# Kernel optimization log

Hardware: AMD Instinct MI355X
Metric: run time of the kernel (lower is better)

The kernel has to match this reference:

```python
import jax, jax.numpy as jnp
import numpy as np

INPUT_SIZE = 1024
HEAD_SIZE = 64


def setup_inputs() -> dict:
    key = jax.random.key(0)
    kx, kk, kq, kv = jax.random.split(key, 4)
    B, T, C, H = 4, 4096, INPUT_SIZE, HEAD_SIZE
    x = jax.random.normal(kx, (B, T, C), dtype=jnp.float32)
    # nn.Linear(C, H, bias=False) weight is (H, C); we store transposed (C, H)
    # so that y = x @ W matches torch's x @ weight.T
    scale = 1.0 / np.sqrt(C)
    Wk = jax.random.uniform(kk, (C, H), dtype=jnp.float32, minval=-scale, maxval=scale)
    Wq = jax.random.uniform(kq, (C, H), dtype=jnp.float32, minval=-scale, maxval=scale)
    Wv = jax.random.uniform(kv, (C, H), dtype=jnp.float32, minval=-scale, maxval=scale)
    return {"x": x, "Wk": Wk, "Wq": Wq, "Wv": Wv}


def reference(x, Wk, Wq, Wv):
    B, T, C = x.shape
    k = x @ Wk  # (B, T, H)
    q = x @ Wq
    v = x @ Wv
    H = k.shape[-1]
    # scaled scores (B, T, T)
    wei = jnp.einsum('bth,bsh->bts', q, k) * (H ** -0.5)
    causal = jnp.tril(jnp.ones((T, T), dtype=bool))
    wei = jnp.where(causal, wei, -jnp.inf)
    wei = jax.nn.softmax(wei, axis=-1)
    out = jnp.einsum('bts,bsh->bth', wei, v)  # (B, T, H)
    return out
```

## Files before the change

kernel.cpp:

```cpp
#include <hip/hip_runtime.h>
#include <math.h>


#define BT   16384
#define TDIM 4096
#define CDIM 1024
#define HDIM 64
#define ACCW 68
#define NSLOT 288

typedef __attribute__((ext_vector_type(8))) short bf16x8;
typedef __attribute__((ext_vector_type(4))) float f32x4;
typedef __attribute__((ext_vector_type(8))) unsigned short us8;
typedef __attribute__((ext_vector_type(4))) unsigned short us4;

static __device__ __forceinline__ unsigned short f2bf(float f) {
    unsigned int u = __float_as_uint(f);
    u += 0x7fffu + ((u >> 16) & 1u);
    return (unsigned short)(u >> 16);
}

static __device__ __forceinline__ void pswap(unsigned &x, unsigned &y) {
    asm("v_permlane32_swap_b32 %0, %1" : "+v"(x), "+v"(y));
    asm("v_permlane16_swap_b32 %0, %1" : "+v"(x), "+v"(y));
}

__global__ __launch_bounds__(256) void wtrans(
    const float* __restrict__ Wk, const float* __restrict__ Wq,
    const float* __restrict__ Wv, unsigned short* __restrict__ wtg)
{
    int idx = blockIdx.x * 256 + threadIdx.x;
    int mat = idx >> 16;
    int rem = idx & 65535;
    int h = rem >> 10, c = rem & 1023;
    const float* W = (mat == 0) ? Wk : (mat == 1) ? Wq : Wv;
    wtg[idx] = f2bf(W[c * HDIM + h]);
}

__global__ __launch_bounds__(512) void qkv_proj(
    const float* __restrict__ x, const unsigned short* __restrict__ wtg,
    unsigned short* __restrict__ kg, unsigned short* __restrict__ qg,
    unsigned short* __restrict__ vtg)
{
    __shared__ __align__(16) unsigned short xs[2][32][72];
    __shared__ __align__(16) unsigned short wts[2][192][72];
    const int t = threadIdx.x;
    const int lane = t & 63, wv = t >> 6, quad = lane >> 4, l16 = lane & 15;
    const int mt = wv >> 2;
    const int nq = wv & 3;
    const int row0 = blockIdx.x * 32;

    const int xr = t >> 4, xc4 = (t & 15) * 4;
    const int wn = t >> 3, wc8 = (t & 7) * 8;

    f32x4 acc3[3];
    #pragma unroll
    for (int i = 0; i < 3; i++) acc3[i] = (f32x4){0.f, 0.f, 0.f, 0.f};

    const size_t xrow = (size_t)(row0 + xr) * CDIM + xc4;

    float4 xv = *(const float4*)&x[xrow];
    us8 w0 = *(const us8*)&wtg[(size_t)(wn +   0) * CDIM + wc8];
    us8 w1 = *(const us8*)&wtg[(size_t)(wn +  64) * CDIM + wc8];
    us8 w2 = *(const us8*)&wtg[(size_t)(wn + 128) * CDIM + wc8];
    {
        us4 pk = { f2bf(xv.x), f2bf(xv.y), f2bf(xv.z), f2bf(xv.w) };
        *(us4*)&xs[0][xr][xc4] = pk;
        *(us8*)&wts[0][wn +   0][wc8] = w0;
        *(us8*)&wts[0][wn +  64][wc8] = w1;
        *(us8*)&wts[0][wn + 128][wc8] = w2;
    }
    xv = *(const float4*)&x[xrow + 64];
    w0 = *(const us8*)&wtg[(size_t)(wn +   0) * CDIM + 64 + wc8];
    w1 = *(const us8*)&wtg[(size_t)(wn +  64) * CDIM + 64 + wc8];
    w2 = *(const us8*)&wtg[(size_t)(wn + 128) * CDIM + 64 + wc8];
    __syncthreads();

    for (int it = 0; it < 16; it++) {
        const int buf = it & 1;
        if (it + 1 < 16) {
            us4 pk = { f2bf(xv.x), f2bf(xv.y), f2bf(xv.z), f2bf(xv.w) };
            *(us4*)&xs[buf ^ 1][xr][xc4] = pk;
            *(us8*)&wts[buf ^ 1][wn +   0][wc8] = w0;
            *(us8*)&wts[buf ^ 1][wn +  64][wc8] = w1;
            *(us8*)&wts[buf ^ 1][wn + 128][wc8] = w2;
            if (it + 2 < 16) {
                int nc = (it + 2) * 64;
                xv = *(const float4*)&x[xrow + nc];
                w0 = *(const us8*)&wtg[(size_t)(wn +   0) * CDIM + nc + wc8];
                w1 = *(const us8*)&wtg[(size_t)(wn +  64) * CDIM + nc + wc8];
                w2 = *(const us8*)&wtg[(size_t)(wn + 128) * CDIM + nc + wc8];
            }
        }
        bf16x8 a0 = *(const bf16x8*)&xs[buf][mt * 16 + l16][quad * 8];
        bf16x8 a1 = *(const bf16x8*)&xs[buf][mt * 16 + l16][32 + quad * 8];
        #pragma unroll
        for (int j = 0; j < 3; j++) {
            int nt = nq * 3 + j;
            bf16x8 b0 = *(const bf16x8*)&wts[buf][nt * 16 + l16][quad * 8];
            bf16x8 b1 = *(const bf16x8*)&wts[buf][nt * 16 + l16][32 + quad * 8];
            acc3[j] = __builtin_amdgcn_mfma_f32_16x16x32_bf16(a0, b0, acc3[j], 0, 0, 0);
            acc3[j] = __builtin_amdgcn_mfma_f32_16x16x32_bf16(a1, b1, acc3[j], 0, 0, 0);
        }
        __syncthreads();
    }

    const int mrow = row0 + mt * 16 + quad * 4;
    #pragma unroll
    for (int j = 0; j < 3; j++) {
        int nt = nq * 3 + j;
        int mat = nt >> 2;
        int col = (nt & 3) * 16 + l16;
        if (mat == 2) {
            int bb = mrow >> 12, tr = mrow & 4095;
            us4 pv = { f2bf(acc3[j][0]), f2bf(acc3[j][1]),
                       f2bf(acc3[j][2]), f2bf(acc3[j][3]) };
            *(us4*)&vtg[((size_t)(bb * HDIM + col) << 12) + tr] = pv;
        } else {
            float s = (mat == 1) ? 0.125f : 1.0f;
            unsigned short* dst = (mat == 0) ? kg : qg;
            #pragma unroll
            for (int reg = 0; reg < 4; reg++)
                dst[(size_t)(mrow + reg) * HDIM + col] = f2bf(acc3[j][reg] * s);
        }
    }
}

__global__ __launch_bounds__(256) void attn(
    const unsigned short* __restrict__ qg, const unsigned short* __restrict__ kg,
    const unsigned short* __restrict__ vtg, float* __restrict__ slabs)
{
    __shared__ __align__(16) unsigned short Ks[2][64][72];
    __shared__ __align__(16) unsigned short Vt[2][64][72];

    const int t = threadIdx.x;
    const int lane = t & 63, wv = t >> 6, quad = lane >> 4, l16 = lane & 15;

    const int b = blockIdx.x / NSLOT;
    const int s = blockIdx.x - b * NSLOT;
    int a;
    if      (s < 8)   a = 0;
    else if (s < 24)  a = 1;
    else if (s < 48)  a = 2;
    else if (s < 80)  a = 3;
    else if (s < 120) a = 4;
    else if (s < 168) a = 5;
    else if (s < 224) a = 6;
    else              a = 7;
    const int u  = s - 4 * a * (a + 1);
    const int qt = a * 8 + u / (a + 1);
    const int c  = u % (a + 1);

    const size_t bbase = (size_t)b * TDIM;
    const int Q0 = qt * 64;
    const int kt0 = c * 8;
    const int kt1 = (kt0 + 7 < qt) ? kt0 + 7 : qt;

    const int qrow = Q0 + wv * 16 + l16;
    const bf16x8 qa0 = *(const bf16x8*)&qg[(bbase + qrow) * HDIM + quad * 8];
    const bf16x8 qa1 = *(const bf16x8*)&qg[(bbase + qrow) * HDIM + 32 + quad * 8];

    const short onev = (l16 == 0) ? (short)0x3F80 : (short)0;
    const bf16x8 ones = { onev, onev, onev, onev, onev, onev, onev, onev };

    f32x4 O[5];
    #pragma unroll
    for (int i = 0; i < 5; i++) O[i] = (f32x4){0.f, 0.f, 0.f, 0.f};

    const int fr = t >> 3, fc = (t & 7) * 8;

    us8 kr0 = *(const us8*)&kg[(bbase + kt0 * 64 + fr) * HDIM + fc];
    us8 kr1 = *(const us8*)&kg[(bbase + kt0 * 64 + fr + 32) * HDIM + fc];
    us8 vr0 = *(const us8*)&vtg[((size_t)(b * HDIM + fr) << 12) + kt0 * 64 + fc];
    us8 vr1 = *(const us8*)&vtg[((size_t)(b * HDIM + fr + 32) << 12) + kt0 * 64 + fc];
    *(us8*)&Ks[0][fr][fc] = kr0;
    *(us8*)&Ks[0][fr + 32][fc] = kr1;
    *(us8*)&Vt[0][fr][fc] = vr0;
    *(us8*)&Vt[0][fr + 32][fc] = vr1;
    if (kt0 < kt1) {
        int kn = kt0 + 1;
        kr0 = *(const us8*)&kg[(bbase + kn * 64 + fr) * HDIM + fc];
        kr1 = *(const us8*)&kg[(bbase + kn * 64 + fr + 32) * HDIM + fc];
        vr0 = *(const us8*)&vtg[((size_t)(b * HDIM + fr) << 12) + kn * 64 + fc];
        vr1 = *(const us8*)&vtg[((size_t)(b * HDIM + fr + 32) << 12) + kn * 64 + fc];
    }
    __syncthreads();

    const int qloc = wv * 16 + l16;
    int buf = 0;
    for (int kt = kt0; kt <= kt1; kt++) {
        f32x4 sT[4];
        #pragma unroll
        for (int st = 0; st < 4; st++) {
            bf16x8 kb0 = *(const bf16x8*)&Ks[buf][st * 16 + l16][quad * 8];
            bf16x8 kb1 = *(const bf16x8*)&Ks[buf][st * 16 + l16][32 + quad * 8];
            f32x4 z = (f32x4){0.f, 0.f, 0.f, 0.f};
            z = __builtin_amdgcn_mfma_f32_16x16x32_bf16(kb0, qa0, z, 0, 0, 0);
            z = __builtin_amdgcn_mfma_f32_16x16x32_bf16(kb1, qa1, z, 0, 0, 0);
            sT[st] = z;
        }

        if (kt < kt1) {
            *(us8*)&Ks[buf ^ 1][fr][fc] = kr0;
            *(us8*)&Ks[buf ^ 1][fr + 32][fc] = kr1;
            *(us8*)&Vt[buf ^ 1][fr][fc] = vr0;
            *(us8*)&Vt[buf ^ 1][fr + 32][fc] = vr1;
            if (kt + 1 < kt1) {
                int kn = kt + 2;
                kr0 = *(const us8*)&kg[(bbase + kn * 64 + fr) * HDIM + fc];
                kr1 = *(const us8*)&kg[(bbase + kn * 64 + fr + 32) * HDIM + fc];
                vr0 = *(const us8*)&vtg[((size_t)(b * HDIM + fr) << 12) + kn * 64 + fc];
                vr1 = *(const us8*)&vtg[((size_t)(b * HDIM + fr + 32) << 12) + kn * 64 + fc];
            }
        }

        float p[4][4];
        if (kt == qt) {
            #pragma unroll
            for (int st = 0; st < 4; st++)
                #pragma unroll
                for (int r = 0; r < 4; r++) {
                    int kkloc = st * 16 + quad * 4 + r;
                    p[st][r] = (kkloc > qloc) ? 0.f : __expf(sT[st][r]);
                }
        } else {
            #pragma unroll
            for (int st = 0; st < 4; st++)
                #pragma unroll
                for (int r = 0; r < 4; r++)
                    p[st][r] = __expf(sT[st][r]);
        }

        unsigned cpk[4][2];
        #pragma unroll
        for (int st = 0; st < 4; st++) {
            asm("v_cvt_pk_bf16_f32 %0, %1, %2"
                : "=v"(cpk[st][0]) : "v"(p[st][0]), "v"(p[st][1]));
            asm("v_cvt_pk_bf16_f32 %0, %1, %2"
                : "=v"(cpk[st][1]) : "v"(p[st][2]), "v"(p[st][3]));
        }
        union { unsigned u[4]; bf16x8 v; } pa0u, pa1u;
        {
            unsigned a0 = cpk[0][0], b0 = cpk[1][0]; pswap(a0, b0);
            unsigned a1 = cpk[0][1], b1 = cpk[1][1]; pswap(a1, b1);
            pa0u.u[0] = a0; pa0u.u[1] = a1; pa0u.u[2] = b0; pa0u.u[3] = b1;
            unsigned a2 = cpk[2][0], b2 = cpk[3][0]; pswap(a2, b2);
            unsigned a3 = cpk[2][1], b3 = cpk[3][1]; pswap(a3, b3);
            pa1u.u[0] = a2; pa1u.u[1] = a3; pa1u.u[2] = b2; pa1u.u[3] = b3;
        }
        const bf16x8 pa0 = pa0u.v, pa1 = pa1u.v;

        #pragma unroll
        for (int nt = 0; nt < 4; nt++) {
            bf16x8 vb0 = *(const bf16x8*)&Vt[buf][nt * 16 + l16][quad * 8];
            bf16x8 vb1 = *(const bf16x8*)&Vt[buf][nt * 16 + l16][32 + quad * 8];
            O[nt] = __builtin_amdgcn_mfma_f32_16x16x32_bf16(pa0, vb0, O[nt], 0, 0, 0);
            O[nt] = __builtin_amdgcn_mfma_f32_16x16x32_bf16(pa1, vb1, O[nt], 0, 0, 0);
        }
        O[4] = __builtin_amdgcn_mfma_f32_16x16x32_bf16(pa0, ones, O[4], 0, 0, 0);
        O[4] = __builtin_amdgcn_mfma_f32_16x16x32_bf16(pa1, ones, O[4], 0, 0, 0);

        __syncthreads();
        buf ^= 1;
    }

    float* slab = slabs + (size_t)(b * NSLOT + s) * 64 * ACCW;
    const int rl = wv * 16 + quad * 4;
    #pragma unroll
    for (int nt = 0; nt < 4; nt++)
        #pragma unroll
        for (int r = 0; r < 4; r++)
            slab[(size_t)(rl + r) * ACCW + nt * 16 + l16] = O[nt][r];
    if (l16 == 0) {
        #pragma unroll
        for (int r = 0; r < 4; r++)
            slab[(size_t)(rl + r) * ACCW + 64] = O[4][r];
    }
}

__global__ __launch_bounds__(256) void reduce_norm(
    const float* __restrict__ slabs, float* __restrict__ out)
{
    int idx = blockIdx.x * 256 + threadIdx.x;
    int row = idx >> 4, c4 = (idx & 15) * 4;
    int b = row >> 12, qt = (row >> 6) & 63, r64 = row & 63;
    int a = qt >> 3, nc = a + 1;
    int base = 4 * a * (a + 1) + (qt & 7) * nc;

    const float* sl = slabs + ((size_t)(b * NSLOT + base) * 64 + r64) * ACCW;
    float4 o = make_float4(0.f, 0.f, 0.f, 0.f);
    float l = 0.f;
    for (int i = 0; i < nc; i++) {
        float4 v = *(const float4*)&sl[c4];
        o.x += v.x; o.y += v.y; o.z += v.z; o.w += v.w;
        l += sl[64];
        sl += (size_t)64 * ACCW;
    }
    float inv = 1.f / l;
    *(float4*)&out[(size_t)row * HDIM + c4] =
        make_float4(o.x * inv, o.y * inv, o.z * inv, o.w * inv);
}

extern "C" void kernel_launch(void* const* d_in, const int* in_sizes, int n_in,
                              void* d_out, int out_size, void* d_ws, size_t ws_size,
                              hipStream_t stream) {
    const float* x  = (const float*)d_in[0];
    const float* Wk = (const float*)d_in[1];
    const float* Wq = (const float*)d_in[2];
    const float* Wv = (const float*)d_in[3];
    float* out = (float*)d_out;

    unsigned short* wtg = (unsigned short*)d_ws;
    unsigned short* kg  = wtg + 196608;
    unsigned short* qg  = kg + (size_t)BT * HDIM;
    unsigned short* vtg = qg + (size_t)BT * HDIM;
    float* slabs = (float*)(vtg + (size_t)4 * HDIM * TDIM);

    wtrans<<<768, 256, 0, stream>>>(Wk, Wq, Wv, wtg);
    qkv_proj<<<BT / 32, 512, 0, stream>>>(x, wtg, kg, qg, vtg);
    attn<<<4 * NSLOT, 256, 0, stream>>>(qg, kg, vtg, slabs);
    reduce_norm<<<BT * HDIM / (4 * 256), 256, 0, stream>>>(slabs, out);
}
```

Baseline: 141.9 us.

## Process 128 query rows per attention block and retile QKV projection

The attention kernel now handles two 64-row query tiles per block, so each K/V tile loaded into shared memory feeds both query groups. The work split changes to 4 key tiles per chunk, with a new slot decomposition found by a small search loop, and the reduction kernel is updated to match. The projection kernel moves to 256 threads with a 32-wide K step, where each wave computes two M tiles that share B operands, and occupancy hints are added to both kernels. The trade-off is higher register pressure from the doubled accumulators, plus a different load balance across blocks.

```diff
diff --git a/kernel.cpp b/kernel.cpp
--- a/kernel.cpp
+++ b/kernel.cpp
@@ -7,7 +7,7 @@
 #define CDIM 1024
 #define HDIM 64
 #define ACCW 68
-#define NSLOT 288
+#define NSLOT 272
 
 typedef __attribute__((ext_vector_type(8))) short bf16x8;
 typedef __attribute__((ext_vector_type(4))) float f32x4;
@@ -37,96 +37,100 @@
     wtg[idx] = f2bf(W[c * HDIM + h]);
 }
 
-__global__ __launch_bounds__(512) void qkv_proj(
+__global__ __launch_bounds__(256, 4) void qkv_proj(
     const float* __restrict__ x, const unsigned short* __restrict__ wtg,
     unsigned short* __restrict__ kg, unsigned short* __restrict__ qg,
     unsigned short* __restrict__ vtg)
 {
-    __shared__ __align__(16) unsigned short xs[2][32][72];
-    __shared__ __align__(16) unsigned short wts[2][192][72];
+    __shared__ __align__(16) unsigned short xs[2][32][36];
+    __shared__ __align__(16) unsigned short wts[2][192][36];
     const int t = threadIdx.x;
     const int lane = t & 63, wv = t >> 6, quad = lane >> 4, l16 = lane & 15;
-    const int mt = wv >> 2;
-    const int nq = wv & 3;
     const int row0 = blockIdx.x * 32;
 
-    const int xr = t >> 4, xc4 = (t & 15) * 4;
-    const int wn = t >> 3, wc8 = (t & 7) * 8;
-
-    f32x4 acc3[3];
+    const int xr = t >> 3, xc4 = (t & 7) * 4;
+    const int wr0 = t >> 2,          wc0 = (t & 3) * 8;
+    const int wr1 = (t + 256) >> 2,  wc1 = wc0;
+    const int wr2 = (t + 512) >> 2,  wc2 = wc0;
+
+    f32x4 acc[2][3];
     #pragma unroll
-    for (int i = 0; i < 3; i++) acc3[i] = (f32x4){0.f, 0.f, 0.f, 0.f};
+    for (int m = 0; m < 2; m++)
+        #pragma unroll
+        for (int j = 0; j < 3; j++) acc[m][j] = (f32x4){0.f, 0.f, 0.f, 0.f};
 
     const size_t xrow = (size_t)(row0 + xr) * CDIM + xc4;
 
     float4 xv = *(const float4*)&x[xrow];
-    us8 w0 = *(const us8*)&wtg[(size_t)(wn +   0) * CDIM + wc8];
-    us8 w1 = *(const us8*)&wtg[(size_t)(wn +  64) * CDIM + wc8];
-    us8 w2 = *(const us8*)&wtg[(size_t)(wn + 128) * CDIM + wc8];
+    us8 w0 = *(const us8*)&wtg[(size_t)wr0 * CDIM + wc0];
+    us8 w1 = *(const us8*)&wtg[(size_t)wr1 * CDIM + wc1];
+    us8 w2 = *(const us8*)&wtg[(size_t)wr2 * CDIM + wc2];
     {
         us4 pk = { f2bf(xv.x), f2bf(xv.y), f2bf(xv.z), f2bf(xv.w) };
         *(us4*)&xs[0][xr][xc4] = pk;
-        *(us8*)&wts[0][wn +   0][wc8] = w0;
-        *(us8*)&wts[0][wn +  64][wc8] = w1;
-        *(us8*)&wts[0][wn + 128][wc8] = w2;
-    }
-    xv = *(const float4*)&x[xrow + 64];
-    w0 = *(const us8*)&wtg[(size_t)(wn +   0) * CDIM + 64 + wc8];
-    w1 = *(const us8*)&wtg[(size_t)(wn +  64) * CDIM + 64 + wc8];
-    w2 = *(const us8*)&wtg[(size_t)(wn + 128) * CDIM + 64 + wc8];
+        *(us8*)&wts[0][wr0][wc0] = w0;
+        *(us8*)&wts[0][wr1][wc1] = w1;
+        *(us8*)&wts[0][wr2][wc2] = w2;
+    }
+    xv = *(const float4*)&x[xrow + 32];
+    w0 = *(const us8*)&wtg[(size_t)wr0 * CDIM + 32 + wc0];
+    w1 = *(const us8*)&wtg[(size_t)wr1 * CDIM + 32 + wc1];
+    w2 = *(const us8*)&wtg[(size_t)wr2 * CDIM + 32 + wc2];
     __syncthreads();
 
-    for (int it = 0; it < 16; it++) {
+    for (int it = 0; it < 32; it++) {
         const int buf = it & 1;
-        if (it + 1 < 16) {
+        if (it + 1 < 32) {
             us4 pk = { f2bf(xv.x), f2bf(xv.y), f2bf(xv.z), f2bf(xv.w) };
             *(us4*)&xs[buf ^ 1][xr][xc4] = pk;
-            *(us8*)&wts[buf ^ 1][wn +   0][wc8] = w0;
-            *(us8*)&wts[buf ^ 1][wn +  64][wc8] = w1;
-            *(us8*)&wts[buf ^ 1][wn + 128][wc8] = w2;
-            if (it + 2 < 16) {
-                int nc = (it + 2) * 64;
+            *(us8*)&wts[buf ^ 1][wr0][wc0] = w0;
+            *(us8*)&wts[buf ^ 1][wr1][wc1] = w1;
+            *(us8*)&wts[buf ^ 1][wr2][wc2] = w2;
+            if (it + 2 < 32) {
+                int nc = (it + 2) * 32;
                 xv = *(const float4*)&x[xrow + nc];
-                w0 = *(const us8*)&wtg[(size_t)(wn +   0) * CDIM + nc + wc8];
-                w1 = *(const us8*)&wtg[(size_t)(wn +  64) * CDIM + nc + wc8];
-                w2 = *(const us8*)&wtg[(size_t)(wn + 128) * CDIM + nc + wc8];
-            }
-        }
-        bf16x8 a0 = *(const bf16x8*)&xs[buf][mt * 16 + l16][quad * 8];
-        bf16x8 a1 = *(const bf16x8*)&xs[buf][mt * 16 + l16][32 + quad * 8];
+                w0 = *(const us8*)&wtg[(size_t)wr0 * CDIM + nc + wc0];
+                w1 = *(const us8*)&wtg[(size_t)wr1 * CDIM + nc + wc1];
+                w2 = *(const us8*)&wtg[(size_t)wr2 * CDIM + nc + wc2];
+            }
+        }
+        bf16x8 a0 = *(const bf16x8*)&xs[buf][l16][quad * 8];
+        bf16x8 a1 = *(const bf16x8*)&xs[buf][16 + l16][quad * 8];
         #pragma unroll
         for (int j = 0; j < 3; j++) {
-            int nt = nq * 3 + j;
-            bf16x8 b0 = *(const bf16x8*)&wts[buf][nt * 16 + l16][quad * 8];
-            bf16x8 b1 = *(const bf16x8*)&wts[buf][nt * 16 + l16][32 + quad * 8];
-            acc3[j] = __builtin_amdgcn_mfma_f32_16x16x32_bf16(a0, b0, acc3[j], 0, 0, 0);
-            acc3[j] = __builtin_amdgcn_mfma_f32_16x16x32_bf16(a1, b1, acc3[j], 0, 0, 0);
+            int nt = wv * 3 + j;
+            bf16x8 bb = *(const bf16x8*)&wts[buf][nt * 16 + l16][quad * 8];
+            acc[0][j] = __builtin_amdgcn_mfma_f32_16x16x32_bf16(a0, bb, acc[0][j], 0, 0, 0);
+            acc[1][j] = __builtin_amdgcn_mfma_f32_16x16x32_bf16(a1, bb, acc[1][j], 0, 0, 0);
         }
         __syncthreads();
     }
 
-    const int mrow = row0 + mt * 16 + quad * 4;
     #pragma unroll
-    for (int j = 0; j < 3; j++) {
-        int nt = nq * 3 + j;
-        int mat = nt >> 2;
-        int col = (nt & 3) * 16 + l16;
-        if (mat == 2) {
-            int bb = mrow >> 12, tr = mrow & 4095;
-            us4 pv = { f2bf(acc3[j][0]), f2bf(acc3[j][1]),
-                       f2bf(acc3[j][2]), f2bf(acc3[j][3]) };
-            *(us4*)&vtg[((size_t)(bb * HDIM + col) << 12) + tr] = pv;
-        } else {
-            float s = (mat == 1) ? 0.125f : 1.0f;
-            unsigned short* dst = (mat == 0) ? kg : qg;
-            #pragma unroll
-            for (int reg = 0; reg < 4; reg++)
-                dst[(size_t)(mrow + reg) * HDIM + col] = f2bf(acc3[j][reg] * s);
-        }
-    }
-}
-
-__global__ __launch_bounds__(256) void attn(
+    for (int mt = 0; mt < 2; mt++) {
+        const int mrow = row0 + mt * 16 + quad * 4;
+        #pragma unroll
+        for (int j = 0; j < 3; j++) {
+            int nt = wv * 3 + j;
+            int mat = nt >> 2;
+            int col = (nt & 3) * 16 + l16;
+            if (mat == 2) {
+                int bb = mrow >> 12, tr = mrow & 4095;
+                us4 pv = { f2bf(acc[mt][j][0]), f2bf(acc[mt][j][1]),
+                           f2bf(acc[mt][j][2]), f2bf(acc[mt][j][3]) };
+                *(us4*)&vtg[((size_t)(bb * HDIM + col) << 12) + tr] = pv;
+            } else {
+                float s = (mat == 1) ? 0.125f : 1.0f;
+                unsigned short* dst = (mat == 0) ? kg : qg;
+                #pragma unroll
+                for (int reg = 0; reg < 4; reg++)
+                    dst[(size_t)(mrow + reg) * HDIM + col] = f2bf(acc[mt][j][reg] * s);
+            }
+        }
+    }
+}
+
+__global__ __launch_bounds__(256, 3) void attn(
     const unsigned short* __restrict__ qg, const unsigned short* __restrict__ kg,
     const unsigned short* __restrict__ vtg, float* __restrict__ slabs)
 {
@@ -138,34 +142,31 @@
 
     const int b = blockIdx.x / NSLOT;
     const int s = blockIdx.x - b * NSLOT;
-    int a;
-    if      (s < 8)   a = 0;
-    else if (s < 24)  a = 1;
-    else if (s < 48)  a = 2;
-    else if (s < 80)  a = 3;
-    else if (s < 120) a = 4;
-    else if (s < 168) a = 5;
-    else if (s < 224) a = 6;
-    else              a = 7;
-    const int u  = s - 4 * a * (a + 1);
-    const int qt = a * 8 + u / (a + 1);
-    const int c  = u % (a + 1);
+    int i = 0;
+    while ((((i + 2) * (i + 2)) >> 2) <= s) ++i;
+    const int c = s - (((i + 1) * (i + 1)) >> 2);
 
     const size_t bbase = (size_t)b * TDIM;
-    const int Q0 = qt * 64;
-    const int kt0 = c * 8;
-    const int kt1 = (kt0 + 7 < qt) ? kt0 + 7 : qt;
-
-    const int qrow = Q0 + wv * 16 + l16;
-    const bf16x8 qa0 = *(const bf16x8*)&qg[(bbase + qrow) * HDIM + quad * 8];
-    const bf16x8 qa1 = *(const bf16x8*)&qg[(bbase + qrow) * HDIM + 32 + quad * 8];
+    const int Q0 = i * 128;
+    const int kt0 = c * 4;
+    const int ktmax = 2 * i + 1;
+    const int kt1 = (kt0 + 3 < ktmax) ? kt0 + 3 : ktmax;
+
+    const int qr = Q0 + wv * 16 + l16;
+    bf16x8 qa0[2], qa1[2];
+    qa0[0] = *(const bf16x8*)&qg[(bbase + qr) * HDIM + quad * 8];
+    qa1[0] = *(const bf16x8*)&qg[(bbase + qr) * HDIM + 32 + quad * 8];
+    qa0[1] = *(const bf16x8*)&qg[(bbase + qr + 64) * HDIM + quad * 8];
+    qa1[1] = *(const bf16x8*)&qg[(bbase + qr + 64) * HDIM + 32 + quad * 8];
 
     const short onev = (l16 == 0) ? (short)0x3F80 : (short)0;
     const bf16x8 ones = { onev, onev, onev, onev, onev, onev, onev, onev };
 
-    f32x4 O[5];
+    f32x4 O[2][5];
     #pragma unroll
-    for (int i = 0; i < 5; i++) O[i] = (f32x4){0.f, 0.f, 0.f, 0.f};
+    for (int g = 0; g < 2; g++)
+        #pragma unroll
+        for (int n = 0; n < 5; n++) O[g][n] = (f32x4){0.f, 0.f, 0.f, 0.f};
 
     const int fr = t >> 3, fc = (t & 7) * 8;
 
@@ -189,15 +190,14 @@
     const int qloc = wv * 16 + l16;
     int buf = 0;
     for (int kt = kt0; kt <= kt1; kt++) {
-        f32x4 sT[4];
+        const int d = kt - 2 * i;
+        const bool do0 = (d < 1);
+
+        bf16x8 kb0[4], kb1[4];
         #pragma unroll
         for (int st = 0; st < 4; st++) {
-            bf16x8 kb0 = *(const bf16x8*)&Ks[buf][st * 16 + l16][quad * 8];
-            bf16x8 kb1 = *(const bf16x8*)&Ks[buf][st * 16 + l16][32 + quad * 8];
-            f32x4 z = (f32x4){0.f, 0.f, 0.f, 0.f};
-            z = __builtin_amdgcn_mfma_f32_16x16x32_bf16(kb0, qa0, z, 0, 0, 0);
-            z = __builtin_amdgcn_mfma_f32_16x16x32_bf16(kb1, qa1, z, 0, 0, 0);
-            sT[st] = z;
+            kb0[st] = *(const bf16x8*)&Ks[buf][st * 16 + l16][quad * 8];
+            kb1[st] = *(const bf16x8*)&Ks[buf][st * 16 + l16][32 + quad * 8];
         }
 
         if (kt < kt1) {
@@ -214,67 +214,89 @@
             }
         }
 
-        float p[4][4];
-        if (kt == qt) {
+        bf16x8 pa0[2], pa1[2];
+        #pragma unroll
+        for (int g = 0; g < 2; g++) {
+            if (g == 0 && !do0) continue;
+            f32x4 sT[4];
             #pragma unroll
-            for (int st = 0; st < 4; st++)
+            for (int st = 0; st < 4; st++) {
+                f32x4 z = (f32x4){0.f, 0.f, 0.f, 0.f};
+                z = __builtin_amdgcn_mfma_f32_16x16x32_bf16(kb0[st], qa0[g], z, 0, 0, 0);
+                z = __builtin_amdgcn_mfma_f32_16x16x32_bf16(kb1[st], qa1[g], z, 0, 0, 0);
+                sT[st] = z;
+            }
+            const bool diag = (d == g);
+            float p[4][4];
+            if (diag) {
                 #pragma unroll
-                for (int r = 0; r < 4; r++) {
-                    int kkloc = st * 16 + quad * 4 + r;
-                    p[st][r] = (kkloc > qloc) ? 0.f : __expf(sT[st][r]);
-                }
-        } else {
+                for (int st = 0; st < 4; st++)
+                    #pragma unroll
+                    for (int r = 0; r < 4; r++) {
+                        int kkloc = st * 16 + quad * 4 + r;
+                        p[st][r] = (kkloc > qloc) ? 0.f : __expf(sT[st][r]);
+                    }
+            } else {
+                #pragma unroll
+                for (int st = 0; st < 4; st++)
+                    #pragma unroll
+                    for (int r = 0; r < 4; r++)
+                        p[st][r] = __expf(sT[st][r]);
+            }
+            unsigned cpk[4][2];
             #pragma unroll
-            for (int st = 0; st < 4; st++)
-                #pragma unroll
-                for (int r = 0; r < 4; r++)
-                    p[st][r] = __expf(sT[st][r]);
-        }
-
-        unsigned cpk[4][2];
-        #pragma unroll
-        for (int st = 0; st < 4; st++) {
-            asm("v_cvt_pk_bf16_f32 %0, %1, %2"
-                : "=v"(cpk[st][0]) : "v"(p[st][0]), "v"(p[st][1]));
-            asm("v_cvt_pk_bf16_f32 %0, %1, %2"
-                : "=v"(cpk[st][1]) : "v"(p[st][2]), "v"(p[st][3]));
-        }
-        union { unsigned u[4]; bf16x8 v; } pa0u, pa1u;
-        {
+            for (int st = 0; st < 4; st++) {
+                asm("v_cvt_pk_bf16_f32 %0, %1, %2"
+                    : "=v"(cpk[st][0]) : "v"(p[st][0]), "v"(p[st][1]));
+                asm("v_cvt_pk_bf16_f32 %0, %1, %2"
+                    : "=v"(cpk[st][1]) : "v"(p[st][2]), "v"(p[st][3]));
+            }
+            union { unsigned u[4]; bf16x8 v; } u0, u1;
             unsigned a0 = cpk[0][0], b0 = cpk[1][0]; pswap(a0, b0);
             unsigned a1 = cpk[0][1], b1 = cpk[1][1]; pswap(a1, b1);
-            pa0u.u[0] = a0; pa0u.u[1] = a1; pa0u.u[2] = b0; pa0u.u[3] = b1;
+            u0.u[0] = a0; u0.u[1] = a1; u0.u[2] = b0; u0.u[3] = b1;
             unsigned a2 = cpk[2][0], b2 = cpk[3][0]; pswap(a2, b2);
             unsigned a3 = cpk[2][1], b3 = cpk[3][1]; pswap(a3, b3);
-            pa1u.u[0] = a2; pa1u.u[1] = a3; pa1u.u[2] = b2; pa1u.u[3] = b3;
-        }
-        const bf16x8 pa0 = pa0u.v, pa1 = pa1u.v;
+            u1.u[0] = a2; u1.u[1] = a3; u1.u[2] = b2; u1.u[3] = b3;
+            pa0[g] = u0.v; pa1[g] = u1.v;
+        }
 
         #pragma unroll
         for (int nt = 0; nt < 4; nt++) {
             bf16x8 vb0 = *(const bf16x8*)&Vt[buf][nt * 16 + l16][quad * 8];
             bf16x8 vb1 = *(const bf16x8*)&Vt[buf][nt * 16 + l16][32 + quad * 8];
-            O[nt] = __builtin_amdgcn_mfma_f32_16x16x32_bf16(pa0, vb0, O[nt], 0, 0, 0);
-            O[nt] = __builtin_amdgcn_mfma_f32_16x16x32_bf16(pa1, vb1, O[nt], 0, 0, 0);
-        }
-        O[4] = __builtin_amdgcn_mfma_f32_16x16x32_bf16(pa0, ones, O[4], 0, 0, 0);
-        O[4] = __builtin_amdgcn_mfma_f32_16x16x32_bf16(pa1, ones, O[4], 0, 0, 0);
+            if (do0) {
+                O[0][nt] = __builtin_amdgcn_mfma_f32_16x16x32_bf16(pa0[0], vb0, O[0][nt], 0, 0, 0);
+                O[0][nt] = __builtin_amdgcn_mfma_f32_16x16x32_bf16(pa1[0], vb1, O[0][nt], 0, 0, 0);
+            }
+            O[1][nt] = __builtin_amdgcn_mfma_f32_16x16x32_bf16(pa0[1], vb0, O[1][nt], 0, 0, 0);
+            O[1][nt] = __builtin_amdgcn_mfma_f32_16x16x32_bf16(pa1[1], vb1, O[1][nt], 0, 0, 0);
+        }
+        if (do0) {
+            O[0][4] = __builtin_amdgcn_mfma_f32_16x16x32_bf16(pa0[0], ones, O[0][4], 0, 0, 0);
+            O[0][4] = __builtin_amdgcn_mfma_f32_16x16x32_bf16(pa1[0], ones, O[0][4], 0, 0, 0);
+        }
+        O[1][4] = __builtin_amdgcn_mfma_f32_16x16x32_bf16(pa0[1], ones, O[1][4], 0, 0, 0);
+        O[1][4] = __builtin_amdgcn_mfma_f32_16x16x32_bf16(pa1[1], ones, O[1][4], 0, 0, 0);
 
         __syncthreads();
         buf ^= 1;
     }
 
-    float* slab = slabs + (size_t)(b * NSLOT + s) * 64 * ACCW;
-    const int rl = wv * 16 + quad * 4;
+    float* slab = slabs + (size_t)(b * NSLOT + s) * 128 * ACCW;
     #pragma unroll
-    for (int nt = 0; nt < 4; nt++)
-        #pragma unroll
-        for (int r = 0; r < 4; r++)
-            slab[(size_t)(rl + r) * ACCW + nt * 16 + l16] = O[nt][r];
-    if (l16 == 0) {
-        #pragma unroll
-        for (int r = 0; r < 4; r++)
-            slab[(size_t)(rl + r) * ACCW + 64] = O[4][r];
+    for (int g = 0; g < 2; g++) {
+        const int rl = g * 64 + wv * 16 + quad * 4;
+        #pragma unroll
+        for (int nt = 0; nt < 4; nt++)
+            #pragma unroll
+            for (int r = 0; r < 4; r++)
+                slab[(size_t)(rl + r) * ACCW + nt * 16 + l16] = O[g][nt][r];
+        if (l16 == 0) {
+            #pragma unroll
+            for (int r = 0; r < 4; r++)
+                slab[(size_t)(rl + r) * ACCW + 64] = O[g][4][r];
+        }
     }
 }
 
@@ -283,18 +305,18 @@
 {
     int idx = blockIdx.x * 256 + threadIdx.x;
     int row = idx >> 4, c4 = (idx & 15) * 4;
-    int b = row >> 12, qt = (row >> 6) & 63, r64 = row & 63;
-    int a = qt >> 3, nc = a + 1;
-    int base = 4 * a * (a + 1) + (qt & 7) * nc;
-
-    const float* sl = slabs + ((size_t)(b * NSLOT + base) * 64 + r64) * ACCW;
+    int b = row >> 12, i = (row >> 7) & 31, r128 = row & 127;
+    int nc = (i + 2) >> 1;
+    int base = ((i + 1) * (i + 1)) >> 2;
+
+    const float* sl = slabs + ((size_t)(b * NSLOT + base) * 128 + r128) * ACCW;
     float4 o = make_float4(0.f, 0.f, 0.f, 0.f);
     float l = 0.f;
-    for (int i = 0; i < nc; i++) {
+    for (int k = 0; k < nc; k++) {
         float4 v = *(const float4*)&sl[c4];
         o.x += v.x; o.y += v.y; o.z += v.z; o.w += v.w;
         l += sl[64];
-        sl += (size_t)64 * ACCW;
+        sl += (size_t)128 * ACCW;
     }
     float inv = 1.f / l;
     *(float4*)&out[(size_t)row * HDIM + c4] =
@@ -317,7 +339,7 @@
     float* slabs = (float*)(vtg + (size_t)4 * HDIM * TDIM);
 
     wtrans<<<768, 256, 0, stream>>>(Wk, Wq, Wv, wtg);
-    qkv_proj<<<BT / 32, 512, 0, stream>>>(x, wtg, kg, qg, vtg);
+    qkv_proj<<<BT / 32, 256, 0, stream>>>(x, wtg, kg, qg, vtg);
     attn<<<4 * NSLOT, 256, 0, stream>>>(qg, kg, vtg, slabs);
     reduce_norm<<<BT * HDIM / (4 * 256), 256, 0, stream>>>(slabs, out);
 }
```

Result: slower. 151.4 us (+6.7%).
